# Performance work log

Measured on AMD Instinct MI355X. Metric: run time of the kernel, lower is better.

The kernel has to match this reference:

```python
import jax, jax.numpy as jnp
import numpy as np

B, N = 2, 8192


def setup_inputs() -> dict:
    key = jax.random.key(0)
    ks = jax.random.split(key, 12)
    p = lambda k: jax.random.normal(k, (1, 1), jnp.float32) * 0.5
    return {
        "x": jax.random.normal(ks[0], (B, N), jnp.float32),
        "DSM": jax.random.uniform(ks[1], (N, N), jnp.float32),
        "w1": p(ks[2]), "b1": jnp.zeros((1,), jnp.float32),
        "lw1": p(ks[3]), "lb1": jnp.zeros((1,), jnp.float32),
        "lw2": p(ks[4]), "lb2": jnp.zeros((1,), jnp.float32),
        "w2": p(ks[5]), "b2": jnp.zeros((1,), jnp.float32),
        "w3": p(ks[6]), "b3": jnp.zeros((1,), jnp.float32),
        "wa": p(ks[7]), "ba": jnp.zeros((1,), jnp.float32),
        "wv": p(ks[8]), "bv": jnp.zeros((1,), jnp.float32),
    }


def _gcn_weighted(h, adj, w, b):
    # PyG GCNConv(normalize=True) on a complete graph whose edge weights are
    # adj[src, dst]; all self-loops already exist, so add_remaining_self_loops
    # is a no-op. deg[c] = sum over incoming edge weights (column sum),
    # norm[r,c] = deg[r]^-1/2 * adj[r,c] * deg[c]^-1/2, scatter-add at targets.
    deg = jnp.sum(adj, axis=0)                              # [N]
    dinv = jnp.where(deg > 0, jax.lax.rsqrt(deg), 0.0)
    anorm = dinv[:, None] * adj * dinv[None, :]             # [src, dst]
    hw = h * w[0, 0]                                        # Linear(1,1,bias=False)
    out = jnp.einsum('rc,brd->bcd', anorm, hw)              # [B,N,1]
    return out + b


def _gcn_uniform(h, w, b):
    # edge_weight=None on the complete graph: deg = N everywhere, every
    # normalized edge weight = 1/N -> output at each node is the node-mean.
    m = jnp.mean(h * w[0, 0], axis=-2, keepdims=True)       # [B,1,1]
    return jnp.broadcast_to(m, h.shape) + b


def reference(x, DSM, w1, b1, lw1, lb1, lw2, lb2, w2, b2, w3, b3, wa, ba, wv, bv):
    h = x[:, :, None]                                       # [B,N,1]
    h = jax.nn.relu(_gcn_weighted(h, DSM, w1, b1))
    h = jax.nn.relu(h * lw1[0, 0] + lb1)
    h = jax.nn.relu(h * lw2[0, 0] + lb2)
    h = jax.nn.relu(_gcn_uniform(h, w2, b2))
    h = jax.nn.relu(_gcn_uniform(h, w3, b3))
    action_prob = jax.nn.softmax(h * wa[0, 0] + ba, axis=-1)  # [B,N,1]
    u = jnp.max(h, axis=0, keepdims=True)                   # MaxAggregation dim=0
    v = jnp.max(u, axis=-2, keepdims=True)                  # MaxAggregation dim=-2
    state_values = v * wv[0, 0] + bv                        # [1,1,1]
    return action_prob, state_values
```

## Files before the change

kernel.cpp:

```cpp
#include <hip/hip_runtime.h>
#include <math.h>

#define N 8192
#define NV4 (N / 4)
#define RPB 32
#define NBY (N / RPB)
#define GRID_X 8
#define THREADS 256

typedef float f4 __attribute__((ext_vector_type(4)));

#define DEGP_OFF  0
#define TPART_OFF (NBY * N)
#define DINV_OFF  (TPART_OFF + NBY * 2 * N)
#define G0_OFF    (DINV_OFF + N)
#define G1_OFF    (G0_OFF + N)
#define HPART_OFF (G1_OFF + N)

__global__ void k_colsum(const float* __restrict__ dsm, float* __restrict__ degp) {
    int chunk = (blockIdx.x + blockIdx.y) & (GRID_X - 1);
    int c4 = chunk * THREADS + threadIdx.x;
    int r0 = blockIdx.y * RPB;
    const f4* p = (const f4*)dsm + (size_t)r0 * NV4 + c4;
    f4 acc = 0.f;
#pragma unroll 8
    for (int i = 0; i < RPB; ++i) acc += p[(size_t)i * NV4];
    __builtin_nontemporal_store(acc, (f4*)(degp + (size_t)blockIdx.y * N) + c4);
}

__global__ void k_dinv(const float* __restrict__ degp, const float* __restrict__ x,
                       float* __restrict__ dinvg, float* __restrict__ g0,
                       float* __restrict__ g1) {
    __shared__ float sred[4][64];
    int c0 = blockIdx.x * 64;
    int cl = threadIdx.x & 63;
    int q  = threadIdx.x >> 6;
    const float* dp = degp + c0 + cl;
    float s = 0.f;
#pragma unroll 8
    for (int j = 0; j < NBY / 4; ++j) s += dp[(size_t)(q * (NBY / 4) + j) * N];
    sred[q][cl] = s;
    __syncthreads();
    if (threadIdx.x < 64) {
        int c = c0 + threadIdx.x;
        float d = sred[0][threadIdx.x] + sred[1][threadIdx.x] +
                  sred[2][threadIdx.x] + sred[3][threadIdx.x];
        float di = d > 0.f ? rsqrtf(d) : 0.f;
        dinvg[c] = di;
        g0[c] = di * x[c];
        g1[c] = di * x[N + c];
    }
}

__global__ void k_matvec(const float* __restrict__ dsm, const float* __restrict__ g0,
                         const float* __restrict__ g1, float* __restrict__ tpart) {
    __shared__ float sg0[RPB];
    __shared__ float sg1[RPB];
    int r0 = blockIdx.y * RPB;
    if (threadIdx.x < RPB) {
        sg0[threadIdx.x] = g0[r0 + threadIdx.x];
        sg1[threadIdx.x] = g1[r0 + threadIdx.x];
    }
    __syncthreads();
    int chunk = (blockIdx.x + blockIdx.y) & (GRID_X - 1);
    int c4 = chunk * THREADS + threadIdx.x;
    const f4* p = (const f4*)dsm + (size_t)r0 * NV4 + c4;
    f4 a0 = 0.f, a1 = 0.f;
#pragma unroll 8
    for (int i = 0; i < RPB; ++i) {
        f4 v = p[(size_t)i * NV4];
        a0 += v * sg0[i];
        a1 += v * sg1[i];
    }
    __builtin_nontemporal_store(a0, (f4*)(tpart + ((size_t)blockIdx.y * 2 + 0) * N) + c4);
    __builtin_nontemporal_store(a1, (f4*)(tpart + ((size_t)blockIdx.y * 2 + 1) * N) + c4);
}

__global__ void k_head(const float* __restrict__ dinvg, const float* __restrict__ tpart,
                       const float* __restrict__ w1, const float* __restrict__ b1,
                       const float* __restrict__ lw1, const float* __restrict__ lb1,
                       const float* __restrict__ lw2, const float* __restrict__ lb2,
                       float* __restrict__ hpart, float* __restrict__ out) {
    __shared__ float swred[8];
    int c = blockIdx.x * THREADS + threadIdx.x;

    float t0 = 0.f, t1 = 0.f;
#pragma unroll 8
    for (int by = 0; by < NBY; ++by) {
        t0 += tpart[((size_t)by * 2 + 0) * N + c];
        t1 += tpart[((size_t)by * 2 + 1) * N + c];
    }
    float di = dinvg[c];

    float W1 = w1[0], B1 = b1[0];
    float LW1 = lw1[0], LB1 = lb1[0];
    float LW2 = lw2[0], LB2 = lb2[0];
    float h0 = fmaxf(W1 * di * t0 + B1, 0.f);
    h0 = fmaxf(h0 * LW1 + LB1, 0.f);
    h0 = fmaxf(h0 * LW2 + LB2, 0.f);
    float h1 = fmaxf(W1 * di * t1 + B1, 0.f);
    h1 = fmaxf(h1 * LW1 + LB1, 0.f);
    h1 = fmaxf(h1 * LW2 + LB2, 0.f);

    out[c] = 1.0f;
    out[N + c] = 1.0f;

    float v0 = h0, v1 = h1;
    for (int off = 32; off > 0; off >>= 1) {
        v0 += __shfl_down(v0, off);
        v1 += __shfl_down(v1, off);
    }
    int wave = threadIdx.x >> 6;
    if ((threadIdx.x & 63) == 0) { swred[wave] = v0; swred[4 + wave] = v1; }
    __syncthreads();
    if (threadIdx.x == 0) {
        hpart[blockIdx.x * 2 + 0] = swred[0] + swred[1] + swred[2] + swred[3];
        hpart[blockIdx.x * 2 + 1] = swred[4] + swred[5] + swred[6] + swred[7];
    }
}

__global__ void k_out(const float* __restrict__ hpart,
                      const float* __restrict__ w2, const float* __restrict__ b2,
                      const float* __restrict__ w3, const float* __restrict__ b3,
                      const float* __restrict__ wv, const float* __restrict__ bv,
                      float* __restrict__ out) {
    int tid = threadIdx.x;
    float s0 = tid < 32 ? hpart[tid * 2 + 0] : 0.f;
    float s1 = tid < 32 ? hpart[tid * 2 + 1] : 0.f;
    for (int off = 16; off > 0; off >>= 1) {
        s0 += __shfl_down(s0, off);
        s1 += __shfl_down(s1, off);
    }
    if (tid == 0) {
        float m0 = s0 * (1.0f / (float)N);
        float m1 = s1 * (1.0f / (float)N);
        float a = fmaxf(m0 * w2[0] + b2[0], 0.f);
        a = fmaxf(a * w3[0] + b3[0], 0.f);
        float b = fmaxf(m1 * w2[0] + b2[0], 0.f);
        b = fmaxf(b * w3[0] + b3[0], 0.f);
        float vmax = fmaxf(a, b);
        out[2 * N] = vmax * wv[0] + bv[0];
    }
}

extern "C" void kernel_launch(void* const* d_in, const int* in_sizes, int n_in,
                              void* d_out, int out_size, void* d_ws, size_t ws_size,
                              hipStream_t stream) {
    const float* x   = (const float*)d_in[0];
    const float* dsm = (const float*)d_in[1];
    const float* w1  = (const float*)d_in[2];
    const float* b1  = (const float*)d_in[3];
    const float* lw1 = (const float*)d_in[4];
    const float* lb1 = (const float*)d_in[5];
    const float* lw2 = (const float*)d_in[6];
    const float* lb2 = (const float*)d_in[7];
    const float* w2  = (const float*)d_in[8];
    const float* b2  = (const float*)d_in[9];
    const float* w3  = (const float*)d_in[10];
    const float* b3  = (const float*)d_in[11];
    const float* wv  = (const float*)d_in[14];
    const float* bv  = (const float*)d_in[15];

    float* ws    = (float*)d_ws;
    float* degp  = ws + DEGP_OFF;
    float* tpart = ws + TPART_OFF;
    float* dinvg = ws + DINV_OFF;
    float* g0    = ws + G0_OFF;
    float* g1    = ws + G1_OFF;
    float* hpart = ws + HPART_OFF;

    dim3 big(GRID_X, NBY);
    k_colsum<<<big, THREADS, 0, stream>>>(dsm, degp);
    k_dinv<<<N / 64, THREADS, 0, stream>>>(degp, x, dinvg, g0, g1);
    k_matvec<<<big, THREADS, 0, stream>>>(dsm, g0, g1, tpart);
    k_head<<<N / THREADS, THREADS, 0, stream>>>(dinvg, tpart, w1, b1, lw1, lb1,
                                                lw2, lb2, hpart, (float*)d_out);
    k_out<<<1, 64, 0, stream>>>(hpart, w2, b2, w3, b3, wv, bv, (float*)d_out);
}
```

Baseline: 470.8 us.

## Double rows per block, use cached stores, split head kernel per batch

Raises rows per block from 32 to 64, which halves the partial-sum buffers written by the column-sum and matvec kernels and the work the reduction kernels must read back. Nontemporal stores are replaced with plain stores so the partials may stay in cache for the next kernel. The degree reduction now uses narrower blocks with eight row groups, and the head kernel gets a second grid dimension for the batch index to spread the reduction over more blocks. The trade-off is fewer blocks in the two streaming passes over the matrix, which may reduce memory-level parallelism.

```diff
diff --git a/kernel.cpp b/kernel.cpp
--- a/kernel.cpp
+++ b/kernel.cpp
@@ -3,7 +3,7 @@
 
 #define N 8192
 #define NV4 (N / 4)
-#define RPB 32
+#define RPB 64
 #define NBY (N / RPB)
 #define GRID_X 8
 #define THREADS 256
@@ -25,26 +25,27 @@
     f4 acc = 0.f;
 #pragma unroll 8
     for (int i = 0; i < RPB; ++i) acc += p[(size_t)i * NV4];
-    __builtin_nontemporal_store(acc, (f4*)(degp + (size_t)blockIdx.y * N) + c4);
+    ((f4*)(degp + (size_t)blockIdx.y * N))[c4] = acc;
 }
 
 __global__ void k_dinv(const float* __restrict__ degp, const float* __restrict__ x,
                        float* __restrict__ dinvg, float* __restrict__ g0,
                        float* __restrict__ g1) {
-    __shared__ float sred[4][64];
-    int c0 = blockIdx.x * 64;
-    int cl = threadIdx.x & 63;
-    int q  = threadIdx.x >> 6;
+    __shared__ float sred[8][32];
+    int c0 = blockIdx.x * 32;
+    int cl = threadIdx.x & 31;
+    int q  = threadIdx.x >> 5;
     const float* dp = degp + c0 + cl;
     float s = 0.f;
 #pragma unroll 8
-    for (int j = 0; j < NBY / 4; ++j) s += dp[(size_t)(q * (NBY / 4) + j) * N];
+    for (int j = 0; j < NBY / 8; ++j) s += dp[(size_t)(q * (NBY / 8) + j) * N];
     sred[q][cl] = s;
     __syncthreads();
-    if (threadIdx.x < 64) {
+    if (threadIdx.x < 32) {
         int c = c0 + threadIdx.x;
-        float d = sred[0][threadIdx.x] + sred[1][threadIdx.x] +
-                  sred[2][threadIdx.x] + sred[3][threadIdx.x];
+        float d = 0.f;
+#pragma unroll
+        for (int q2 = 0; q2 < 8; ++q2) d += sred[q2][threadIdx.x];
         float di = d > 0.f ? rsqrtf(d) : 0.f;
         dinvg[c] = di;
         g0[c] = di * x[c];
@@ -72,8 +73,8 @@
         a0 += v * sg0[i];
         a1 += v * sg1[i];
     }
-    __builtin_nontemporal_store(a0, (f4*)(tpart + ((size_t)blockIdx.y * 2 + 0) * N) + c4);
-    __builtin_nontemporal_store(a1, (f4*)(tpart + ((size_t)blockIdx.y * 2 + 1) * N) + c4);
+    ((f4*)(tpart + ((size_t)blockIdx.y * 2 + 0) * N))[c4] = a0;
+    ((f4*)(tpart + ((size_t)blockIdx.y * 2 + 1) * N))[c4] = a1;
 }
 
 __global__ void k_head(const float* __restrict__ dinvg, const float* __restrict__ tpart,
@@ -81,42 +82,29 @@
                        const float* __restrict__ lw1, const float* __restrict__ lb1,
                        const float* __restrict__ lw2, const float* __restrict__ lb2,
                        float* __restrict__ hpart, float* __restrict__ out) {
-    __shared__ float swred[8];
+    __shared__ float swred[4];
     int c = blockIdx.x * THREADS + threadIdx.x;
+    int b = blockIdx.y;
 
-    float t0 = 0.f, t1 = 0.f;
+    const float* tp = tpart + (size_t)b * N + c;
+    float t = 0.f;
 #pragma unroll 8
-    for (int by = 0; by < NBY; ++by) {
-        t0 += tpart[((size_t)by * 2 + 0) * N + c];
-        t1 += tpart[((size_t)by * 2 + 1) * N + c];
-    }
+    for (int by = 0; by < NBY; ++by) t += tp[(size_t)by * 2 * N];
     float di = dinvg[c];
 
-    float W1 = w1[0], B1 = b1[0];
-    float LW1 = lw1[0], LB1 = lb1[0];
-    float LW2 = lw2[0], LB2 = lb2[0];
-    float h0 = fmaxf(W1 * di * t0 + B1, 0.f);
-    h0 = fmaxf(h0 * LW1 + LB1, 0.f);
-    h0 = fmaxf(h0 * LW2 + LB2, 0.f);
-    float h1 = fmaxf(W1 * di * t1 + B1, 0.f);
-    h1 = fmaxf(h1 * LW1 + LB1, 0.f);
-    h1 = fmaxf(h1 * LW2 + LB2, 0.f);
+    float h = fmaxf(w1[0] * di * t + b1[0], 0.f);
+    h = fmaxf(h * lw1[0] + lb1[0], 0.f);
+    h = fmaxf(h * lw2[0] + lb2[0], 0.f);
 
-    out[c] = 1.0f;
-    out[N + c] = 1.0f;
+    out[(size_t)b * N + c] = 1.0f;
 
-    float v0 = h0, v1 = h1;
-    for (int off = 32; off > 0; off >>= 1) {
-        v0 += __shfl_down(v0, off);
-        v1 += __shfl_down(v1, off);
-    }
+    float v = h;
+    for (int off = 32; off > 0; off >>= 1) v += __shfl_down(v, off);
     int wave = threadIdx.x >> 6;
-    if ((threadIdx.x & 63) == 0) { swred[wave] = v0; swred[4 + wave] = v1; }
+    if ((threadIdx.x & 63) == 0) swred[wave] = v;
     __syncthreads();
-    if (threadIdx.x == 0) {
-        hpart[blockIdx.x * 2 + 0] = swred[0] + swred[1] + swred[2] + swred[3];
-        hpart[blockIdx.x * 2 + 1] = swred[4] + swred[5] + swred[6] + swred[7];
-    }
+    if (threadIdx.x == 0)
+        hpart[b * 32 + blockIdx.x] = swred[0] + swred[1] + swred[2] + swred[3];
 }
 
 __global__ void k_out(const float* __restrict__ hpart,
@@ -125,8 +113,8 @@
                       const float* __restrict__ wv, const float* __restrict__ bv,
                       float* __restrict__ out) {
     int tid = threadIdx.x;
-    float s0 = tid < 32 ? hpart[tid * 2 + 0] : 0.f;
-    float s1 = tid < 32 ? hpart[tid * 2 + 1] : 0.f;
+    float s0 = tid < 32 ? hpart[tid] : 0.f;
+    float s1 = tid < 32 ? hpart[32 + tid] : 0.f;
     for (int off = 16; off > 0; off >>= 1) {
         s0 += __shfl_down(s0, off);
         s1 += __shfl_down(s1, off);
@@ -171,9 +159,10 @@
 
     dim3 big(GRID_X, NBY);
     k_colsum<<<big, THREADS, 0, stream>>>(dsm, degp);
-    k_dinv<<<N / 64, THREADS, 0, stream>>>(degp, x, dinvg, g0, g1);
+    k_dinv<<<N / 32, THREADS, 0, stream>>>(degp, x, dinvg, g0, g1);
     k_matvec<<<big, THREADS, 0, stream>>>(dsm, g0, g1, tpart);
-    k_head<<<N / THREADS, THREADS, 0, stream>>>(dinvg, tpart, w1, b1, lw1, lb1,
-                                                lw2, lb2, hpart, (float*)d_out);
+    k_head<<<dim3(N / THREADS, 2), THREADS, 0, stream>>>(dinvg, tpart, w1, b1,
+                                                         lw1, lb1, lw2, lb2,
+                                                         hpart, (float*)d_out);
     k_out<<<1, 64, 0, stream>>>(hpart, w2, b2, w3, b3, wv, bv, (float*)d_out);
 }
```

Measured after the change: 433.1 us. 1.09x faster.
